# Performance work log

Hardware: AMD Instinct MI355X
Metric: run time of the kernel (lower is better)

Reference implementation:

```python
import jax, jax.numpy as jnp
import numpy as np

B, LQ, LT, D = 16, 576, 512, 768
H, DH = 12, 64
TOPK = 64
GATE_INIT = -4.0
EPS = 1e-5


def _layernorm(x, g, b):
    m = jnp.mean(x, axis=-1, keepdims=True)
    v = jnp.mean(jnp.square(x - m), axis=-1, keepdims=True)
    return (x - m) * jax.lax.rsqrt(v + EPS) * g + b


def setup_inputs() -> dict:
    key = jax.random.key(0)
    ks = jax.random.split(key, 8)
    s = D ** -0.5
    return {
        "x_q": jax.random.normal(ks[0], (B, LQ, D), jnp.float32),
        "x_kv": jax.random.normal(ks[1], (B, LT, D), jnp.float32),
        "kv_attn_mask": jnp.ones((B, LT), jnp.int32),
        "wq": jax.random.normal(ks[2], (D, D), jnp.float32) * s,
        "wk": jax.random.normal(ks[3], (D, D), jnp.float32) * s,
        "wv": jax.random.normal(ks[4], (D, D), jnp.float32) * s,
        "wo": jax.random.normal(ks[5], (D, D), jnp.float32) * s,
        "ln_q_g": jnp.ones((D,), jnp.float32),
        "ln_q_b": jnp.zeros((D,), jnp.float32),
        "ln_kv_g": jnp.ones((D,), jnp.float32),
        "ln_kv_b": jnp.zeros((D,), jnp.float32),
        "head_queries": jax.random.normal(ks[6], (H, DH), jnp.float32) * DH ** -0.5,
        "resid_logit": jnp.asarray(GATE_INIT, jnp.float32),
    }


def reference(x_q, x_kv, kv_attn_mask, wq, wk, wv, wo,
              ln_q_g, ln_q_b, ln_kv_g, ln_kv_b, head_queries, resid_logit):
    scale = DH ** -0.5
    Bc, Lq, _ = x_q.shape
    Lt = x_kv.shape[1]
    xq_n = _layernorm(x_q, ln_q_g, ln_q_b)
    xkv_n = _layernorm(x_kv, ln_kv_g, ln_kv_b)
    # torch Linear: y = x @ W.T
    q = (xq_n @ wq.T).reshape(Bc, Lq, H, DH).transpose(0, 2, 1, 3)   # [B,H,Lq,DH]
    k = (xkv_n @ wk.T).reshape(Bc, Lt, H, DH).transpose(0, 2, 1, 3)  # [B,H,Lt,DH]
    v = (xkv_n @ wv.T).reshape(Bc, Lt, H, DH).transpose(0, 2, 1, 3)

    valid = (kv_attn_mask != 0)  # [B,Lt]
    neg = jnp.asarray(-jnp.inf, q.dtype)

    # head-wise gate from learned head queries attending over keys
    gate_scores = jnp.einsum('hd,bhld->bhl', head_queries, k) * scale  # [B,H,Lt]
    gate_scores = jnp.where(valid[:, None, :], gate_scores, neg)
    gate_attn = jax.nn.softmax(gate_scores, axis=-1)
    c_h = jnp.einsum('bhl,bhld->bhd', gate_attn, k)
    g_logits = jnp.einsum('bhd,hd->bh', c_h, head_queries) * scale
    g_h = jax.nn.sigmoid(g_logits)[:, :, None, None]  # [B,H,1,1]

    # top-k token routing: zero out non-selected K/V (matches torch.where -> zeros)
    if TOPK and TOPK < Lt:
        _, topk_idx = jax.lax.top_k(gate_scores, TOPK)  # [B,H,K]
        keep = jax.nn.one_hot(topk_idx, Lt, dtype=q.dtype).sum(axis=-2) > 0  # [B,H,Lt]
        k = jnp.where(keep[..., None], k, 0.0)
        v = jnp.where(keep[..., None], v, 0.0)

    attn_logits = jnp.einsum('bhqd,bhkd->bhqk', q, k) * scale  # [B,H,Lq,Lt]
    attn_logits = jnp.where(valid[:, None, None, :], attn_logits, neg)
    attn = jax.nn.softmax(attn_logits, axis=-1)
    out = jnp.einsum('bhqk,bhkd->bhqd', attn, v) * g_h
    out = out.transpose(0, 2, 1, 3).reshape(Bc, Lq, H * DH)
    out = out @ wo.T
    alpha = jax.nn.sigmoid(resid_logit)
    return x_q + alpha * out
```

## Files before the change

### kernel.cpp

```cpp
#include <hip/hip_runtime.h>
#include <math.h>

#define BB 16
#define LQ 576
#define LT 512
#define DD 768
#define HH 12
#define DH 64
#define TOPK 64

typedef __attribute__((ext_vector_type(8))) short bf16x8;
typedef __attribute__((ext_vector_type(4))) float f32x4;
typedef __attribute__((ext_vector_type(4))) unsigned short u16x4;

static constexpr size_t XQBF  = 0;
static constexpr size_t XKVBF = 3538944;
static constexpr size_t WQB   = 6684672;
static constexpr size_t WKB   = 6979584;
static constexpr size_t WVB   = 7274496;
static constexpr size_t WOB   = 7569408;
static constexpr size_t QBFo  = 7864320;
static constexpr size_t KBFo  = 11403264;
static constexpr size_t VBFo  = 14548992;
static constexpr size_t IDXo  = 17694720;
static constexpr size_t VBIA  = 17707008;
static constexpr size_t NDVo  = 17719296;
static constexpr size_t GHo   = 17719488;
static constexpr size_t KCo   = 17719680;
static constexpr size_t VCTo  = 18112896;

__device__ inline unsigned short f2bf(float f) {
  union { float f; unsigned u; } v; v.f = f;
  unsigned r = v.u + 0x7FFFu + ((v.u >> 16) & 1u);
  return (unsigned short)(r >> 16);
}
__device__ inline float bf2f(unsigned short u) {
  union { unsigned u; float f; } v; v.u = ((unsigned)u) << 16;
  return v.f;
}
__device__ inline void gload_lds16(const void* src, void* dst) {
  __builtin_amdgcn_global_load_lds((const __attribute__((address_space(1))) void*)src,
                                   (__attribute__((address_space(3))) void*)dst, 16, 0, 0);
}

__global__ __launch_bounds__(256) void ln_all(const float* __restrict__ xq,
                                              const float* __restrict__ xkv,
                                              const float* __restrict__ gq,
                                              const float* __restrict__ bq,
                                              const float* __restrict__ gkv,
                                              const float* __restrict__ bkv,
                                              unsigned short* __restrict__ yq,
                                              unsigned short* __restrict__ ykv) {
  int row = blockIdx.x;
  const float *xr, *gg, *bb;
  unsigned short* yr;
  if (row < BB * LQ) {
    xr = xq + (size_t)row * DD; gg = gq; bb = bq; yr = yq + (size_t)row * DD;
  } else {
    int r = row - BB * LQ;
    xr = xkv + (size_t)r * DD; gg = gkv; bb = bkv; yr = ykv + (size_t)r * DD;
  }
  int t = threadIdx.x;
  float v0 = xr[t], v1 = xr[t + 256], v2 = xr[t + 512];
  __shared__ float red[4];
  float s = v0 + v1 + v2;
  #pragma unroll
  for (int o = 32; o > 0; o >>= 1) s += __shfl_xor(s, o);
  if ((t & 63) == 0) red[t >> 6] = s;
  __syncthreads();
  float m = (red[0] + red[1] + red[2] + red[3]) * (1.0f / 768.0f);
  float d0 = v0 - m, d1 = v1 - m, d2 = v2 - m;
  float s2 = d0 * d0 + d1 * d1 + d2 * d2;
  #pragma unroll
  for (int o = 32; o > 0; o >>= 1) s2 += __shfl_xor(s2, o);
  __syncthreads();
  if ((t & 63) == 0) red[t >> 6] = s2;
  __syncthreads();
  float var = (red[0] + red[1] + red[2] + red[3]) * (1.0f / 768.0f);
  float rs = rsqrtf(var + 1e-5f);
  yr[t]       = f2bf(d0 * rs * gg[t]       + bb[t]);
  yr[t + 256] = f2bf(d1 * rs * gg[t + 256] + bb[t + 256]);
  yr[t + 512] = f2bf(d2 * rs * gg[t + 512] + bb[t + 512]);
}

__global__ __launch_bounds__(256) void conv4(const float* __restrict__ s0, const float* __restrict__ s1,
                                             const float* __restrict__ s2, const float* __restrict__ s3,
                                             unsigned short* d0, unsigned short* d1,
                                             unsigned short* d2, unsigned short* d3) {
  const float* s; unsigned short* d;
  switch (blockIdx.y) {
    case 0: s = s0; d = d0; break;
    case 1: s = s1; d = d1; break;
    case 2: s = s2; d = d2; break;
    default: s = s3; d = d3; break;
  }
  int i = (blockIdx.x * 256 + threadIdx.x) * 4;
  float4 v = *reinterpret_cast<const float4*>(&s[i]);
  u16x4 o = { f2bf(v.x), f2bf(v.y), f2bf(v.z), f2bf(v.w) };
  *reinterpret_cast<u16x4*>(&d[i]) = o;
}


#define GEMM_PREAMBLE()                                                        \
  const int tid = threadIdx.x;                                                 \
  const int w = tid >> 6, l = tid & 63;                                        \
  const int wr = w >> 1, wc = w & 1, lq = l & 15, g = l >> 4;                  \
  const int srow = l >> 3;                                                     \
  const int scol = ((l & 7) * 16) ^ ((srow & 7) << 4);                         \
  int aoff[4][2], boff[4][2];                                                  \
  _Pragma("unroll")                                                            \
  for (int mi = 0; mi < 4; ++mi) {                                             \
    int rowa = wr * 64 + mi * 16 + lq;                                         \
    int rowb = wc * 64 + mi * 16 + lq;                                         \
    _Pragma("unroll")                                                          \
    for (int ks = 0; ks < 2; ++ks) {                                           \
      aoff[mi][ks] = rowa * 64 + (((ks * 64 + g * 16) ^ ((rowa & 7) << 4)) >> 1); \
      boff[mi][ks] = rowb * 64 + (((ks * 64 + g * 16) ^ ((rowb & 7) << 4)) >> 1); \
    }                                                                          \
  }

#define STAGE2(BUFI, T)                                                        \
  {                                                                            \
    int k0s = (T) * 64;                                                        \
    _Pragma("unroll")                                                          \
    for (int it = 0; it < 4; ++it) {                                           \
      int rbase = it * 32 + w * 8;                                             \
      gload_lds16(Asrc + (size_t)rbase * DD + k0s, &As[BUFI][rbase * 64]);     \
      gload_lds16(Bsrc + (size_t)rbase * DD + k0s, &Bs[BUFI][rbase * 64]);     \
    }                                                                          \
  }

#define COMPUTE2(BUFI)                                                         \
  {                                                                            \
    bf16x8 a[4][2], b[4][2];                                                   \
    _Pragma("unroll")                                                          \
    for (int mi = 0; mi < 4; ++mi)                                             \
      _Pragma("unroll")                                                        \
      for (int ks = 0; ks < 2; ++ks) {                                         \
        a[mi][ks] = *reinterpret_cast<const bf16x8*>(&As[BUFI][aoff[mi][ks]]); \
        b[mi][ks] = *reinterpret_cast<const bf16x8*>(&Bs[BUFI][boff[mi][ks]]); \
      }                                                                        \
    _Pragma("unroll")                                                          \
    for (int ks = 0; ks < 2; ++ks)                                             \
      _Pragma("unroll")                                                        \
      for (int mi = 0; mi < 4; ++mi)                                           \
        _Pragma("unroll")                                                      \
        for (int ni = 0; ni < 4; ++ni)                                         \
          acc[mi][ni] = __builtin_amdgcn_mfma_f32_16x16x32_bf16(               \
              a[mi][ks], b[ni][ks], acc[mi][ni], 0, 0, 0);                     \
  }

#define GEMM_KLOOP()                                                           \
  STAGE2(0, 0);                                                                \
  STAGE2(1, 1);                                                                \
  _Pragma("unroll")                                                            \
  for (int t = 0; t < 12; ++t) {                                               \
    if (t < 11) asm volatile("s_waitcnt vmcnt(8)" ::: "memory");               \
    else        asm volatile("s_waitcnt vmcnt(0)" ::: "memory");               \
    __builtin_amdgcn_sched_barrier(0);                                         \
    __builtin_amdgcn_s_barrier();                                              \
    if ((t & 1) == 0) { COMPUTE2(0); } else { COMPUTE2(1); }                   \
    __builtin_amdgcn_s_barrier();                                              \
    __builtin_amdgcn_sched_barrier(0);                                         \
    if (t + 2 < 12) {                                                          \
      if ((t & 1) == 0) { STAGE2(0, t + 2); } else { STAGE2(1, t + 2); }       \
    }                                                                          \
  }

__global__ __launch_bounds__(256, 2) void qkv_gemm(const unsigned short* __restrict__ xqb,
                                                   const unsigned short* __restrict__ wqb,
                                                   const unsigned short* __restrict__ xkvb,
                                                   const unsigned short* __restrict__ wkvb,
                                                   unsigned short* __restrict__ QBF,
                                                   unsigned short* __restrict__ KBF,
                                                   unsigned short* __restrict__ VBF) {
  __shared__ __align__(16) unsigned short As[2][128 * 64];
  __shared__ __align__(16) unsigned short Bs[2][128 * 64];
  GEMM_PREAMBLE();

  int p = blockIdx.x;
  int bid = (p & 7) * 150 + (p >> 3);
  const unsigned short *A, *W;
  unsigned short* dst;
  int mtile, nt;
  float scale;
  if (bid < 432) {
    A = xqb; W = wqb; mtile = bid / 6; nt = bid % 6; dst = QBF; scale = 0.125f;
  } else {
    int q = bid - 432;
    A = xkvb; W = wkvb; mtile = q / 12; nt = q % 12; scale = 1.0f;
    dst = (nt < 6) ? KBF : VBF;
  }
  const int bm = mtile * 128, bn = nt * 128;
  const unsigned short* Asrc = A + (size_t)(bm + srow) * DD + (scol >> 1);
  const unsigned short* Bsrc = W + (size_t)(bn + srow) * DD + (scol >> 1);

  f32x4 acc[4][4] = {};
  GEMM_KLOOP();

  const int m_base = bm + wr * 64;
  const int n_base = (bn + wc * 64) - ((bid >= 432 && nt >= 6) ? 768 : 0);
  #pragma unroll
  for (int mi = 0; mi < 4; ++mi)
    #pragma unroll
    for (int r = 0; r < 4; ++r) {
      int m = m_base + mi * 16 + g * 4 + r;
      #pragma unroll
      for (int ni = 0; ni < 4; ++ni) {
        int n = n_base + ni * 16 + lq;
        dst[(size_t)m * DD + n] = f2bf(acc[mi][ni][r] * scale);
      }
    }
}

__global__ __launch_bounds__(256, 2) void o_gemm(const unsigned short* __restrict__ ABF,
                                                 const unsigned short* __restrict__ wob,
                                                 float* __restrict__ out,
                                                 const float* __restrict__ resid,
                                                 const float* __restrict__ gl) {
  __shared__ __align__(16) unsigned short As[2][128 * 64];
  __shared__ __align__(16) unsigned short Bs[2][128 * 64];
  GEMM_PREAMBLE();

  int p = blockIdx.x;
  int bid = (p & 7) * 54 + (p >> 3);
  const int mtile = bid / 6, nt = bid % 6;
  const int bm = mtile * 128, bn = nt * 128;
  const unsigned short* Asrc = ABF + (size_t)(bm + srow) * DD + (scol >> 1);
  const unsigned short* Bsrc = wob + (size_t)(bn + srow) * DD + (scol >> 1);

  f32x4 acc[4][4] = {};
  GEMM_KLOOP();

  float alpha = 1.0f / (1.0f + __expf(-gl[0]));
  const int m_base = bm + wr * 64, n_base = bn + wc * 64;
  #pragma unroll
  for (int mi = 0; mi < 4; ++mi)
    #pragma unroll
    for (int r = 0; r < 4; ++r) {
      int m = m_base + mi * 16 + g * 4 + r;
      #pragma unroll
      for (int ni = 0; ni < 4; ++ni) {
        int n = n_base + ni * 16 + lq;
        out[(size_t)m * DD + n] = resid[(size_t)m * DD + n] + alpha * acc[mi][ni][r];
      }
    }
}

__global__ __launch_bounds__(512) void gate_topk(const unsigned short* __restrict__ Kbuf,
                                                 const float* __restrict__ hq,
                                                 const int* __restrict__ mask,
                                                 int* __restrict__ idxo,
                                                 float* __restrict__ vbias,
                                                 float* __restrict__ ndv,
                                                 float* __restrict__ g_h) {
  int bh = blockIdx.x, b = bh / HH, h = bh % HH;
  int l = threadIdx.x;
  __shared__ __align__(16) unsigned short Kl[512 * 64];
  __shared__ float s_sc[512];
  __shared__ float s_p[512];
  __shared__ float part[8][64];
  __shared__ float red[8];
  __shared__ int wred[8];
  const float scale = 0.125f;
  const unsigned short* kr = Kbuf + ((size_t)(b * LT + l)) * DD + h * DH;
  float sc = 0.0f;
  #pragma unroll
  for (int j = 0; j < 8; ++j) {
    bf16x8 kk = *reinterpret_cast<const bf16x8*>(kr + j * 8);
    int cj = ((j ^ (l & 7)) * 8);
    *reinterpret_cast<bf16x8*>(&Kl[l * 64 + cj]) = kk;
    #pragma unroll
    for (int e = 0; e < 8; ++e) sc += bf2f((unsigned short)kk[e]) * hq[h * DH + j * 8 + e];
  }
  sc *= scale;
  bool maskv = (mask[b * LT + l] != 0);
  if (!maskv) sc = -INFINITY;
  s_sc[l] = sc;
  __syncthreads();
  float m = sc;
  #pragma unroll
  for (int o = 32; o > 0; o >>= 1) m = fmaxf(m, __shfl_xor(m, o));
  if ((l & 63) == 0) red[l >> 6] = m;
  __syncthreads();
  m = red[0];
  #pragma unroll
  for (int w = 1; w < 8; w++) m = fmaxf(m, red[w]);
  float p = expf(sc - m);
  float ssum = p;
  #pragma unroll
  for (int o = 32; o > 0; o >>= 1) ssum += __shfl_xor(ssum, o);
  __syncthreads();
  if ((l & 63) == 0) red[l >> 6] = ssum;
  __syncthreads();
  float Z = 0.0f;
  #pragma unroll
  for (int w = 0; w < 8; w++) Z += red[w];
  p /= Z;
  s_p[l] = p;
  __syncthreads();
  {
    int d = l & 63, grp = l >> 6;
    int j = d >> 3, e = d & 7;
    float cacc = 0.0f;
    #pragma unroll 4
    for (int i = 0; i < 64; ++i) {
      int t = grp * 64 + i;
      float kv = bf2f(Kl[t * 64 + ((j ^ (t & 7)) * 8) + e]);
      cacc += s_p[t] * kv;
    }
    part[grp][d] = cacc;
  }
  __syncthreads();
  if (l < 64) {
    float c = 0.0f;
    #pragma unroll
    for (int gpi = 0; gpi < 8; ++gpi) c += part[gpi][l];
    float v = c * hq[h * DH + l];
    #pragma unroll
    for (int o = 32; o > 0; o >>= 1) v += __shfl_xor(v, o);
    if (l == 0) g_h[bh] = 1.0f / (1.0f + expf(-v * scale));
  }
  float my = s_sc[l];
  int cnt = 0;
  for (int j = 0; j < LT; j++) {
    float sj = s_sc[j];
    cnt += (sj > my || (sj == my && j < l)) ? 1 : 0;
  }
  if (cnt < TOPK) {
    idxo[bh * TOPK + cnt] = l;
    vbias[bh * TOPK + cnt] = maskv ? 0.0f : -INFINITY;
  }
  int dv = (maskv && cnt >= TOPK) ? 1 : 0;
  unsigned long long bal = __ballot(dv);
  if ((l & 63) == 0) wred[l >> 6] = __popcll(bal);
  __syncthreads();
  if (l == 0) {
    int nd = 0;
    #pragma unroll
    for (int w = 0; w < 8; w++) nd += wred[w];
    ndv[bh] = (float)nd;
  }
}

__global__ __launch_bounds__(256) void compact_kv(const unsigned short* __restrict__ KBF,
                                                  const unsigned short* __restrict__ VBF,
                                                  const int* __restrict__ idxo,
                                                  unsigned short* __restrict__ KC,
                                                  unsigned short* __restrict__ VCT) {
  int bh = blockIdx.x, b = bh / HH, h = bh % HH;
  int tid = threadIdx.x;
  __shared__ int sidx[64];
  __shared__ __align__(16) unsigned short vt[64][80];
  if (tid < 64) sidx[tid] = idxo[bh * TOPK + tid];
  __syncthreads();
  #pragma unroll
  for (int it = 0; it < 2; ++it) {
    int j = it * 32 + (tid >> 3);
    int c = (tid & 7) * 8;
    size_t src = ((size_t)(b * LT) + sidx[j]) * DD + h * DH + c;
    bf16x8 kv = *reinterpret_cast<const bf16x8*>(&KBF[src]);
    *reinterpret_cast<bf16x8*>(&KC[(size_t)bh * 4096 + j * 64 + c]) = kv;
    bf16x8 vv = *reinterpret_cast<const bf16x8*>(&VBF[src]);
    *reinterpret_cast<bf16x8*>(&vt[j][c]) = vv;
  }
  __syncthreads();
  #pragma unroll
  for (int it = 0; it < 2; ++it) {
    int d = it * 32 + (tid >> 3);
    int jc = (tid & 7) * 8;
    bf16x8 o;
    #pragma unroll
    for (int i = 0; i < 8; i++) o[i] = (short)vt[jc + i][d];
    *reinterpret_cast<bf16x8*>(&VCT[(size_t)bh * 4096 + d * 64 + jc]) = o;
  }
}

__global__ __launch_bounds__(256) void attn_topk(const unsigned short* __restrict__ Qb,
                                                 const unsigned short* __restrict__ KC,
                                                 const unsigned short* __restrict__ VCT,
                                                 const float* __restrict__ vbias,
                                                 const float* __restrict__ ndv,
                                                 const float* __restrict__ g_h,
                                                 unsigned short* __restrict__ att) {
  const int bh = blockIdx.y, b = bh / HH, h = bh % HH;
  const int q0 = blockIdx.x * 64;
  const int tid = threadIdx.x;
  const int w = tid >> 6, l = tid & 63;
  const int lq = l & 15, g = l >> 4;

  __shared__ __align__(16) unsigned short Klds[64 * 64];
  __shared__ __align__(16) unsigned short Vlds[64 * 64];
  __shared__ float svb[64];

  const int srow = l >> 3;
  const int scol = ((l & 7) * 16) ^ ((srow & 7) << 4);
  #pragma unroll
  for (int it = 0; it < 2; ++it) {
    int rbase = w * 16 + it * 8;
    gload_lds16(KC  + (size_t)bh * 4096 + (rbase + srow) * 64 + (scol >> 1), &Klds[rbase * 64]);
    gload_lds16(VCT + (size_t)bh * 4096 + (rbase + srow) * 64 + (scol >> 1), &Vlds[rbase * 64]);
  }
  if (tid < 64) svb[tid] = vbias[bh * TOPK + tid];

  bf16x8 qf0, qf1;
  {
    const unsigned short* qrow =
        Qb + ((size_t)(b * LQ + q0 + w * 16 + lq)) * DD + h * DH + g * 8;
    qf0 = *reinterpret_cast<const bf16x8*>(qrow);
    qf1 = *reinterpret_cast<const bf16x8*>(qrow + 32);
  }
  __syncthreads();

  f32x4 S[4];
  #pragma unroll
  for (int kt = 0; kt < 4; ++kt) {
    f32x4 acc = {};
    int row = kt * 16 + lq;
    int c0 = (g * 16) ^ ((row & 7) << 4);
    int c1 = (64 + g * 16) ^ ((row & 7) << 4);
    bf16x8 a0 = *reinterpret_cast<const bf16x8*>(&Klds[row * 64 + (c0 >> 1)]);
    bf16x8 a1 = *reinterpret_cast<const bf16x8*>(&Klds[row * 64 + (c1 >> 1)]);
    acc = __builtin_amdgcn_mfma_f32_16x16x32_bf16(a0, qf0, acc, 0, 0, 0);
    acc = __builtin_amdgcn_mfma_f32_16x16x32_bf16(a1, qf1, acc, 0, 0, 0);
    S[kt] = acc;
  }

  float s_v[16];
  float mx = -INFINITY;
  #pragma unroll
  for (int kt = 0; kt < 4; ++kt)
    #pragma unroll
    for (int r = 0; r < 4; ++r) {
      float s = S[kt][r] + svb[kt * 16 + g * 4 + r];
      s_v[kt * 4 + r] = s;
      mx = fmaxf(mx, s);
    }
  mx = fmaxf(mx, __shfl_xor(mx, 16));
  mx = fmaxf(mx, __shfl_xor(mx, 32));
  float nd = ndv[bh];
  float m2 = (nd > 0.0f) ? fmaxf(mx, 0.0f) : mx;

  float psum = 0.0f;
  unsigned short pb[16];
  #pragma unroll
  for (int i = 0; i < 16; ++i) {
    float p = __expf(s_v[i] - m2);
    psum += p;
    pb[i] = f2bf(p);
  }
  psum += __shfl_xor(psum, 16);
  psum += __shfl_xor(psum, 32);
  float Z = psum + nd * __expf(-m2);
  float inv = 1.0f / Z;

  bf16x8 pa0, pa1;
  #pragma unroll
  for (int j = 0; j < 8; ++j) { pa0[j] = (short)pb[j]; pa1[j] = (short)pb[8 + j]; }

  f32x4 O[4] = {};
  #pragma unroll
  for (int dt = 0; dt < 4; ++dt) {
    int r = dt * 16 + lq;
    int swz = (r & 7) << 4;
    #pragma unroll
    for (int ks = 0; ks < 2; ++ks) {
      int cl = (64 * ks + g * 8) ^ swz;
      int ch = (64 * ks + 32 + g * 8) ^ swz;
      u16x4 lo = *reinterpret_cast<const u16x4*>(&Vlds[r * 64 + (cl >> 1)]);
      u16x4 hi = *reinterpret_cast<const u16x4*>(&Vlds[r * 64 + (ch >> 1)]);
      bf16x8 vb = { (short)lo[0], (short)lo[1], (short)lo[2], (short)lo[3],
                    (short)hi[0], (short)hi[1], (short)hi[2], (short)hi[3] };
      O[dt] = __builtin_amdgcn_mfma_f32_16x16x32_bf16(ks == 0 ? pa0 : pa1, vb, O[dt], 0, 0, 0);
    }
  }

  float invl[4];
  #pragma unroll
  for (int r = 0; r < 4; ++r) invl[r] = __shfl(inv, g * 4 + r);
  float gh = g_h[bh];
  #pragma unroll
  for (int dt = 0; dt < 4; ++dt)
    #pragma unroll
    for (int r = 0; r < 4; ++r) {
      int q = q0 + w * 16 + g * 4 + r;
      att[((size_t)(b * LQ + q)) * DD + h * DH + dt * 16 + lq] =
          f2bf(O[dt][r] * invl[r] * gh);
    }
}

extern "C" void kernel_launch(void* const* d_in, const int* in_sizes, int n_in,
                              void* d_out, int out_size, void* d_ws, size_t ws_size,
                              hipStream_t stream) {
  const float* x_q      = (const float*)d_in[0];
  const float* x_kv     = (const float*)d_in[1];
  const int*   mask     = (const int*)d_in[2];
  const float* wq       = (const float*)d_in[3];
  const float* wk       = (const float*)d_in[4];
  const float* wv       = (const float*)d_in[5];
  const float* wo       = (const float*)d_in[6];
  const float* ln_q_g   = (const float*)d_in[7];
  const float* ln_q_b   = (const float*)d_in[8];
  const float* ln_kv_g  = (const float*)d_in[9];
  const float* ln_kv_b  = (const float*)d_in[10];
  const float* hq       = (const float*)d_in[11];
  const float* resid_l  = (const float*)d_in[12];
  float* out = (float*)d_out;
  float* ws  = (float*)d_ws;

  unsigned short* xqb  = (unsigned short*)(ws + XQBF);
  unsigned short* xkvb = (unsigned short*)(ws + XKVBF);
  unsigned short* wqb  = (unsigned short*)(ws + WQB);
  unsigned short* wkb  = (unsigned short*)(ws + WKB);
  unsigned short* wvb  = (unsigned short*)(ws + WVB);
  unsigned short* wob  = (unsigned short*)(ws + WOB);
  unsigned short* QBF  = (unsigned short*)(ws + QBFo);
  unsigned short* KBF  = (unsigned short*)(ws + KBFo);
  unsigned short* VBF  = (unsigned short*)(ws + VBFo);
  int*            IDX  = (int*)(ws + IDXo);
  unsigned short* KC   = (unsigned short*)(ws + KCo);
  unsigned short* VCT  = (unsigned short*)(ws + VCTo);
  unsigned short* ABF  = xqb;

  conv4<<<dim3(576, 4), dim3(256), 0, stream>>>(wq, wk, wv, wo, wqb, wkb, wvb, wob);

  ln_all<<<dim3(BB * LQ + BB * LT), dim3(256), 0, stream>>>(x_q, x_kv, ln_q_g, ln_q_b,
                                                            ln_kv_g, ln_kv_b, xqb, xkvb);

  qkv_gemm<<<dim3(1200), dim3(256), 0, stream>>>(xqb, wqb, xkvb, wkb, QBF, KBF, VBF);

  gate_topk<<<dim3(BB * HH), dim3(512), 0, stream>>>(KBF, hq, mask, IDX,
                                                     ws + VBIA, ws + NDVo, ws + GHo);

  compact_kv<<<dim3(BB * HH), dim3(256), 0, stream>>>(KBF, VBF, IDX, KC, VCT);

  attn_topk<<<dim3(LQ / 64, BB * HH), dim3(256), 0, stream>>>(QBF, KC, VCT,
                                                              ws + VBIA, ws + NDVo, ws + GHo, ABF);

  o_gemm<<<dim3(432), dim3(256), 0, stream>>>(ABF, wob, out, x_q, resid_l);
}
```

Measured before the change: 118.6 us.

## Compute V only for top-k selected tokens and fuse K compaction into gate

Drops the full V projection from the QKV GEMM so that GEMM covers only Q and K, cutting its tiles from 1200 to 816. A new vc_gemm kernel projects only the 64 selected tokens per (batch, head) straight into the transposed compact layout, using gathered rows of the normalized x_kv. K compaction moves into gate_topk, which writes the selected rows from its LDS copy, so the separate compact_kv kernel is removed. The risk is that vc_gemm runs only 192 small blocks with gathered loads, which may leave the GPU underused.

```diff
diff --git a/kernel.cpp b/kernel.cpp
--- a/kernel.cpp
+++ b/kernel.cpp
@@ -21,7 +21,6 @@
 static constexpr size_t WOB   = 7569408;
 static constexpr size_t QBFo  = 7864320;
 static constexpr size_t KBFo  = 11403264;
-static constexpr size_t VBFo  = 14548992;
 static constexpr size_t IDXo  = 17694720;
 static constexpr size_t VBIA  = 17707008;
 static constexpr size_t NDVo  = 17719296;
@@ -167,19 +166,18 @@
     }                                                                          \
   }
 
-__global__ __launch_bounds__(256, 2) void qkv_gemm(const unsigned short* __restrict__ xqb,
-                                                   const unsigned short* __restrict__ wqb,
-                                                   const unsigned short* __restrict__ xkvb,
-                                                   const unsigned short* __restrict__ wkvb,
-                                                   unsigned short* __restrict__ QBF,
-                                                   unsigned short* __restrict__ KBF,
-                                                   unsigned short* __restrict__ VBF) {
+__global__ __launch_bounds__(256, 2) void qk_gemm(const unsigned short* __restrict__ xqb,
+                                                  const unsigned short* __restrict__ wqb,
+                                                  const unsigned short* __restrict__ xkvb,
+                                                  const unsigned short* __restrict__ wkb,
+                                                  unsigned short* __restrict__ QBF,
+                                                  unsigned short* __restrict__ KBF) {
   __shared__ __align__(16) unsigned short As[2][128 * 64];
   __shared__ __align__(16) unsigned short Bs[2][128 * 64];
   GEMM_PREAMBLE();
 
   int p = blockIdx.x;
-  int bid = (p & 7) * 150 + (p >> 3);
+  int bid = (p & 7) * 102 + (p >> 3);
   const unsigned short *A, *W;
   unsigned short* dst;
   int mtile, nt;
@@ -188,8 +186,7 @@
     A = xqb; W = wqb; mtile = bid / 6; nt = bid % 6; dst = QBF; scale = 0.125f;
   } else {
     int q = bid - 432;
-    A = xkvb; W = wkvb; mtile = q / 12; nt = q % 12; scale = 1.0f;
-    dst = (nt < 6) ? KBF : VBF;
+    A = xkvb; W = wkb; mtile = q / 6; nt = q % 6; dst = KBF; scale = 1.0f;
   }
   const int bm = mtile * 128, bn = nt * 128;
   const unsigned short* Asrc = A + (size_t)(bm + srow) * DD + (scol >> 1);
@@ -198,8 +195,7 @@
   f32x4 acc[4][4] = {};
   GEMM_KLOOP();
 
-  const int m_base = bm + wr * 64;
-  const int n_base = (bn + wc * 64) - ((bid >= 432 && nt >= 6) ? 768 : 0);
+  const int m_base = bm + wr * 64, n_base = bn + wc * 64;
   #pragma unroll
   for (int mi = 0; mi < 4; ++mi)
     #pragma unroll
@@ -253,7 +249,8 @@
                                                  int* __restrict__ idxo,
                                                  float* __restrict__ vbias,
                                                  float* __restrict__ ndv,
-                                                 float* __restrict__ g_h) {
+                                                 float* __restrict__ g_h,
+                                                 unsigned short* __restrict__ KC) {
   int bh = blockIdx.x, b = bh / HH, h = bh % HH;
   int l = threadIdx.x;
   __shared__ __align__(16) unsigned short Kl[512 * 64];
@@ -330,6 +327,11 @@
   if (cnt < TOPK) {
     idxo[bh * TOPK + cnt] = l;
     vbias[bh * TOPK + cnt] = maskv ? 0.0f : -INFINITY;
+    #pragma unroll
+    for (int j = 0; j < 8; ++j) {
+      bf16x8 kk = *reinterpret_cast<const bf16x8*>(&Kl[l * 64 + ((j ^ (l & 7)) * 8)]);
+      *reinterpret_cast<bf16x8*>(&KC[(size_t)bh * 4096 + cnt * 64 + j * 8]) = kk;
+    }
   }
   int dv = (maskv && cnt >= TOPK) ? 1 : 0;
   unsigned long long bal = __ballot(dv);
@@ -343,37 +345,77 @@
   }
 }
 
-__global__ __launch_bounds__(256) void compact_kv(const unsigned short* __restrict__ KBF,
-                                                  const unsigned short* __restrict__ VBF,
+__global__ __launch_bounds__(256, 2) void vc_gemm(const unsigned short* __restrict__ xkvb,
+                                                  const unsigned short* __restrict__ wvb,
                                                   const int* __restrict__ idxo,
-                                                  unsigned short* __restrict__ KC,
                                                   unsigned short* __restrict__ VCT) {
-  int bh = blockIdx.x, b = bh / HH, h = bh % HH;
-  int tid = threadIdx.x;
+  __shared__ __align__(16) unsigned short Xs[2][64 * 64];
+  __shared__ __align__(16) unsigned short Ws[2][64 * 64];
   __shared__ int sidx[64];
-  __shared__ __align__(16) unsigned short vt[64][80];
+  const int bh = blockIdx.x, b = bh / HH, h = bh % HH;
+  const int tid = threadIdx.x;
+  const int w = tid >> 6, l = tid & 63;
+  const int lq = l & 15, g = l >> 4;
   if (tid < 64) sidx[tid] = idxo[bh * TOPK + tid];
   __syncthreads();
-  #pragma unroll
-  for (int it = 0; it < 2; ++it) {
-    int j = it * 32 + (tid >> 3);
-    int c = (tid & 7) * 8;
-    size_t src = ((size_t)(b * LT) + sidx[j]) * DD + h * DH + c;
-    bf16x8 kv = *reinterpret_cast<const bf16x8*>(&KBF[src]);
-    *reinterpret_cast<bf16x8*>(&KC[(size_t)bh * 4096 + j * 64 + c]) = kv;
-    bf16x8 vv = *reinterpret_cast<const bf16x8*>(&VBF[src]);
-    *reinterpret_cast<bf16x8*>(&vt[j][c]) = vv;
-  }
-  __syncthreads();
-  #pragma unroll
-  for (int it = 0; it < 2; ++it) {
-    int d = it * 32 + (tid >> 3);
-    int jc = (tid & 7) * 8;
-    bf16x8 o;
-    #pragma unroll
-    for (int i = 0; i < 8; i++) o[i] = (short)vt[jc + i][d];
-    *reinterpret_cast<bf16x8*>(&VCT[(size_t)bh * 4096 + d * 64 + jc]) = o;
-  }
+  const int srow = l >> 3;
+  const int scol = ((l & 7) * 16) ^ ((srow & 7) << 4);
+  const unsigned short* xsrc0 = xkvb + ((size_t)(b * LT + sidx[w * 16 + srow])) * DD + (scol >> 1);
+  const unsigned short* xsrc1 = xkvb + ((size_t)(b * LT + sidx[w * 16 + 8 + srow])) * DD + (scol >> 1);
+  const unsigned short* wsrc0 = wvb + ((size_t)(h * DH + w * 16 + srow)) * DD + (scol >> 1);
+  const unsigned short* wsrc1 = wvb + ((size_t)(h * DH + w * 16 + 8 + srow)) * DD + (scol >> 1);
+
+#define VC_STAGE(BUFI, T)                                                      \
+  {                                                                            \
+    int k0s = (T) * 64;                                                        \
+    gload_lds16(xsrc0 + k0s, &Xs[BUFI][(w * 16) * 64]);                        \
+    gload_lds16(xsrc1 + k0s, &Xs[BUFI][(w * 16 + 8) * 64]);                    \
+    gload_lds16(wsrc0 + k0s, &Ws[BUFI][(w * 16) * 64]);                        \
+    gload_lds16(wsrc1 + k0s, &Ws[BUFI][(w * 16 + 8) * 64]);                    \
+  }
+
+  f32x4 acc[4] = {};
+
+#define VC_COMPUTE(BUFI)                                                       \
+  {                                                                            \
+    _Pragma("unroll")                                                          \
+    for (int ks = 0; ks < 2; ++ks) {                                           \
+      int arow = w * 16 + lq;                                                  \
+      int acb = (ks * 64 + g * 16) ^ ((arow & 7) << 4);                        \
+      bf16x8 a = *reinterpret_cast<const bf16x8*>(&Ws[BUFI][arow * 64 + (acb >> 1)]); \
+      _Pragma("unroll")                                                        \
+      for (int ni = 0; ni < 4; ++ni) {                                         \
+        int brow = ni * 16 + lq;                                               \
+        int bcb = (ks * 64 + g * 16) ^ ((brow & 7) << 4);                      \
+        bf16x8 bfr = *reinterpret_cast<const bf16x8*>(&Xs[BUFI][brow * 64 + (bcb >> 1)]); \
+        acc[ni] = __builtin_amdgcn_mfma_f32_16x16x32_bf16(a, bfr, acc[ni], 0, 0, 0); \
+      }                                                                        \
+    }                                                                          \
+  }
+
+  VC_STAGE(0, 0);
+  VC_STAGE(1, 1);
+  #pragma unroll
+  for (int t = 0; t < 12; ++t) {
+    if (t < 11) asm volatile("s_waitcnt vmcnt(4)" ::: "memory");
+    else        asm volatile("s_waitcnt vmcnt(0)" ::: "memory");
+    __builtin_amdgcn_sched_barrier(0);
+    __builtin_amdgcn_s_barrier();
+    if ((t & 1) == 0) { VC_COMPUTE(0); } else { VC_COMPUTE(1); }
+    __builtin_amdgcn_s_barrier();
+    __builtin_amdgcn_sched_barrier(0);
+    if (t + 2 < 12) {
+      if ((t & 1) == 0) { VC_STAGE(0, t + 2); } else { VC_STAGE(1, t + 2); }
+    }
+  }
+
+  #pragma unroll
+  for (int ni = 0; ni < 4; ++ni)
+    #pragma unroll
+    for (int r = 0; r < 4; ++r) {
+      int d = w * 16 + g * 4 + r;
+      VCT[(size_t)bh * 4096 + d * 64 + ni * 16 + lq] = f2bf(acc[ni][r]);
+    }
 }
 
 __global__ __launch_bounds__(256) void attn_topk(const unsigned short* __restrict__ Qb,
@@ -516,7 +558,6 @@
   unsigned short* wob  = (unsigned short*)(ws + WOB);
   unsigned short* QBF  = (unsigned short*)(ws + QBFo);
   unsigned short* KBF  = (unsigned short*)(ws + KBFo);
-  unsigned short* VBF  = (unsigned short*)(ws + VBFo);
   int*            IDX  = (int*)(ws + IDXo);
   unsigned short* KC   = (unsigned short*)(ws + KCo);
   unsigned short* VCT  = (unsigned short*)(ws + VCTo);
@@ -527,12 +568,12 @@
   ln_all<<<dim3(BB * LQ + BB * LT), dim3(256), 0, stream>>>(x_q, x_kv, ln_q_g, ln_q_b,
                                                             ln_kv_g, ln_kv_b, xqb, xkvb);
 
-  qkv_gemm<<<dim3(1200), dim3(256), 0, stream>>>(xqb, wqb, xkvb, wkb, QBF, KBF, VBF);
+  qk_gemm<<<dim3(816), dim3(256), 0, stream>>>(xqb, wqb, xkvb, wkb, QBF, KBF);
 
   gate_topk<<<dim3(BB * HH), dim3(512), 0, stream>>>(KBF, hq, mask, IDX,
-                                                     ws + VBIA, ws + NDVo, ws + GHo);
-
-  compact_kv<<<dim3(BB * HH), dim3(256), 0, stream>>>(KBF, VBF, IDX, KC, VCT);
+                                                     ws + VBIA, ws + NDVo, ws + GHo, KC);
+
+  vc_gemm<<<dim3(BB * HH), dim3(256), 0, stream>>>(xkvb, wvb, IDX, VCT);
 
   attn_topk<<<dim3(LQ / 64, BB * HH), dim3(256), 0, stream>>>(QBF, KC, VCT,
                                                               ws + VBIA, ws + NDVo, ws + GHo, ABF);
```

New measurement: 115.7 us. -2.4%, faster.
